# Optimization experiments

Measured on AMD Instinct MI355X. Metric: run time of the kernel, lower is better.

## Reference

```python
import jax, jax.numpy as jnp
import numpy as np
import math

B, S, H = 8, 1024, 768
NH = 12
DH = H // NH


def _linear(x, W, b):
    # torch Linear: y = x @ W.T + b, W: [out, in]
    return jnp.einsum('bsd,ed->bse', x, W) + b


def _split_heads(x):
    # [B,S,H] -> [B,NH,S,DH]
    b, s, _ = x.shape
    return x.reshape(b, s, NH, DH).transpose(0, 2, 1, 3)


def _attend(q, k, v):
    # q,k,v: [B,NH,S,DH]
    scores = jnp.einsum('bhqd,bhkd->bhqk', q, k) / math.sqrt(DH)
    probs = jax.nn.softmax(scores, axis=-1)
    ctx = jnp.einsum('bhqk,bhkd->bhqd', probs, v)
    b, h, s, d = ctx.shape
    return ctx.transpose(0, 2, 1, 3).reshape(b, s, h * d)


def setup_inputs() -> dict:
    key = jax.random.key(0)
    ks = jax.random.split(key, 20)
    sc = 1.0 / math.sqrt(H)
    inp = {
        'hidden_statesx': jax.random.normal(ks[0], (B, S, H), jnp.float32),
        'hidden_statesy': jax.random.normal(ks[1], (B, S, H), jnp.float32),
    }
    names = ['Wq', 'Wk', 'Wv', 'Wo', 'Wqd', 'Wkd', 'Wvd', 'Wod']
    for i, n in enumerate(names):
        inp[n] = jax.random.normal(ks[2 + i], (H, H), jnp.float32) * sc
        inp['b' + n[1:]] = jnp.zeros((H,), jnp.float32)
    inp['w11'] = jnp.full((1,), 0.5, jnp.float32)
    inp['w12'] = jnp.full((1,), 0.5, jnp.float32)
    inp['w21'] = jnp.full((1,), 0.5, jnp.float32)
    inp['w22'] = jnp.full((1,), 0.5, jnp.float32)
    return inp


def reference(hidden_statesx, hidden_statesy,
              Wq, bq, Wk, bk, Wv, bv, Wo, bo,
              Wqd, bqd, Wkd, bkd, Wvd, bvd, Wod, bod,
              w11, w12, w21, w22):
    q = _split_heads(_linear(hidden_statesx, Wq, bq))
    k = _split_heads(_linear(hidden_statesx, Wk, bk))
    v = _split_heads(_linear(hidden_statesx, Wv, bv))
    qd = _split_heads(_linear(hidden_statesy, Wqd, bqd))
    kd = _split_heads(_linear(hidden_statesy, Wkd, bkd))
    vd = _split_heads(_linear(hidden_statesy, Wvd, bvd))

    # self-attention on x and y streams
    attention_sx = _linear(_attend(q, k, v), Wo, bo)
    attention_sy = _linear(_attend(qd, kd, vd), Wod, bod)
    # cross attentions (mba mode)
    attention_cx = _linear(_attend(q, kd, vd), Wo, bo)
    attention_cy = _linear(_attend(qd, k, v), Wod, bod)

    attention_sx = w11 * attention_sx + w12 * attention_cx
    attention_sy = w21 * attention_sy + w22 * attention_cy
    return attention_sx, attention_sy
```

## Files before the change

### kernel.cpp

```cpp
#include <hip/hip_runtime.h>

typedef __bf16 bf16;
typedef __bf16 bf16x8 __attribute__((ext_vector_type(8)));
typedef float f32x4 __attribute__((ext_vector_type(4)));

#define HD 768
#define ELTS 6291456
#define WELTS 589824

__device__ __forceinline__ void gld_lds16(const bf16* g, bf16* l) {
  __builtin_amdgcn_global_load_lds((const __attribute__((address_space(1))) void*)g,
                                   (__attribute__((address_space(3))) void*)l, 16, 0, 0);
}

__device__ __forceinline__ float rdscalar(const void* p, int f) {
  return f ? (float)((const bf16*)p)[0] : ((const float*)p)[0];
}

__device__ __forceinline__ float exp2fast(float x) {
#if __has_builtin(__builtin_amdgcn_exp2f)
  return __builtin_amdgcn_exp2f(x);
#else
  return __builtin_exp2f(x);
#endif
}

__global__ void probe_dtype(const unsigned int* __restrict__ x, int* flag) {
  const int t = threadIdx.x;
  int bad = 0;
#pragma unroll
  for (int i = 0; i < 4; ++i) {
    unsigned int wd = x[t * 4 + i];
    unsigned int e0 = (wd >> 7) & 0xFF;
    unsigned int e1 = (wd >> 23) & 0xFF;
    bad += (e0 >= 134) + (e1 >= 134);
  }
  unsigned long long m = __ballot(bad > 0);
  if (t == 0) *flag = (m == 0ULL) ? 1 : 0;
}

struct CvtArgs {
  const float* src[20];
  bf16* dst[20];
  int n[20];
  const int* flag;
};
__global__ __launch_bounds__(256) void convert_inputs(CvtArgs a) {
  if (*a.flag) return;
  const int seg = blockIdx.y;
  const float* s = a.src[seg];
  bf16* d = a.dst[seg];
  const int n4 = a.n[seg] >> 2;
  for (int i = blockIdx.x * blockDim.x + threadIdx.x; i < n4; i += gridDim.x * blockDim.x) {
    f32x4 v = *(const f32x4*)(s + i * 4);
    bf16 o[4];
#pragma unroll
    for (int e = 0; e < 4; ++e) o[e] = (bf16)v[e];
    *(unsigned long long*)(d + i * 4) = *(unsigned long long*)o;
  }
}

struct GemmArgs {
  const void* A[6];
  const void* Ac[6];
  const void* W[6];
  const void* Wc[6];
  const void* bias[6];
  const void* biasc[6];
  const void* s0[6];
  const void* s1[6];
  void* C[6];
  float cmul[6];
  int c_fixed[6];
  int vt[6];
  int ext_w[6];
  long long out_elem_off[6];
  const int* flag;
};

__global__ __launch_bounds__(256) void gemm_bt(GemmArgs args) {
  const int g = blockIdx.z;
  const int f = *args.flag;
  const bool c_bf = args.c_fixed[g] || f;
  const bool w_f32 = (!f) && args.ext_w[g];
  const bf16* __restrict__ A = (const bf16*)(f ? args.A[g] : args.Ac[g]);
  const void* __restrict__ Wp = f ? args.W[g] : args.Wc[g];
  const void* __restrict__ bias = f ? args.bias[g] : args.biasc[g];
  bf16* Cb = (bf16*)args.C[g] + args.out_elem_off[g];
  float* Cf = (float*)args.C[g] + args.out_elem_off[g];
  float bscale = 1.0f;
  if (args.s0[g]) bscale = rdscalar(args.s0[g], f) + rdscalar(args.s1[g], f);
  const float cmul = args.cmul[g];

  const int m0 = blockIdx.x * 128;
  const int n0 = blockIdx.y * 128;
  const int t = threadIdx.x;
  const int lane = t & 63;
  const int w = t >> 6;
  const int wm = (w >> 1) * 64, wn = (w & 1) * 64;

  __shared__ __attribute__((aligned(16))) bf16 As[128 * 64];
  __shared__ __attribute__((aligned(16))) bf16 Bs[128 * 64];

  f32x4 acc[4][4] = {};

  const int row_s = t >> 3, slot_s = t & 7;
  const int gswz = (slot_s ^ (row_s & 7)) << 3;

  const int fr = lane & 15;
  const int l4 = lane >> 4;
  const int sR0 = ((l4) ^ (fr & 7)) << 3;
  const int sR1 = ((4 + l4) ^ (fr & 7)) << 3;

  for (int kb = 0; kb < 12; ++kb) {
    const int k0 = kb * 64;
#pragma unroll
    for (int i = 0; i < 4; ++i) {
      const int row = row_s + i * 32;
      gld_lds16(A + (size_t)(m0 + row) * HD + k0 + gswz, As + (t + i * 256) * 8);
    }
    if (!w_f32) {
#pragma unroll
      for (int i = 0; i < 4; ++i) {
        const int row = row_s + i * 32;
        gld_lds16((const bf16*)Wp + (size_t)(n0 + row) * HD + k0 + gswz, Bs + (t + i * 256) * 8);
      }
    } else {
      const float* Wf = (const float*)Wp;
#pragma unroll
      for (int i = 0; i < 4; ++i) {
        const int row = row_s + i * 32;
        const size_t src = (size_t)(n0 + row) * HD + k0 + gswz;
        f32x4 u0 = *(const f32x4*)(Wf + src), u1 = *(const f32x4*)(Wf + src + 4);
        bf16x8 v;
#pragma unroll
        for (int e = 0; e < 4; ++e) { v[e] = (bf16)u0[e]; v[e + 4] = (bf16)u1[e]; }
        *(bf16x8*)(Bs + (t + i * 256) * 8) = v;
      }
    }
    __syncthreads();
#pragma unroll
    for (int kk = 0; kk < 2; ++kk) {
      const int sR = kk ? sR1 : sR0;
      bf16x8 af[4], bfr[4];
#pragma unroll
      for (int mi = 0; mi < 4; ++mi)
        af[mi] = *(const bf16x8*)(As + (wm + mi * 16 + fr) * 64 + sR);
#pragma unroll
      for (int ni = 0; ni < 4; ++ni)
        bfr[ni] = *(const bf16x8*)(Bs + (wn + ni * 16 + fr) * 64 + sR);
#pragma unroll
      for (int mi = 0; mi < 4; ++mi)
#pragma unroll
        for (int ni = 0; ni < 4; ++ni)
          acc[mi][ni] = __builtin_amdgcn_mfma_f32_16x16x32_bf16(af[mi], bfr[ni], acc[mi][ni], 0, 0, 0);
    }
    __syncthreads();
  }

  const int rq = (lane >> 4) * 4;
  const int is_vt = args.vt[g];
#pragma unroll
  for (int ni = 0; ni < 4; ++ni) {
    const int col = n0 + wn + ni * 16 + fr;
    const float bv = (w_f32 ? ((const float*)bias)[col]
                            : (float)((const bf16*)bias)[col]) * bscale;
#pragma unroll
    for (int mi = 0; mi < 4; ++mi) {
      const int row = m0 + wm + mi * 16 + rq;
      if (is_vt) {
        const int bb = row >> 10, s = row & 1023;
        const int hh = col >> 6, d = col & 63;
        bf16 tmp[4];
#pragma unroll
        for (int r = 0; r < 4; ++r) tmp[r] = (bf16)((acc[mi][ni][r] + bv) * cmul);
        *(unsigned long long*)(Cb + (((size_t)(bb * 12 + hh)) << 16) + (d << 10) + s) =
            *(const unsigned long long*)tmp;
      } else {
#pragma unroll
        for (int r = 0; r < 4; ++r) {
          const float val = (acc[mi][ni][r] + bv) * cmul;
          if (c_bf) Cb[(size_t)(row + r) * HD + col] = (bf16)val;
          else      Cf[(size_t)(row + r) * HD + col] = val;
        }
      }
    }
  }
}

__global__ __launch_bounds__(256, 4) void attn_mba(
    const bf16* __restrict__ Q, const bf16* __restrict__ Kx, const bf16* __restrict__ Vtx,
    const bf16* __restrict__ Qd, const bf16* __restrict__ Kd, const bf16* __restrict__ Vtd,
    const void* w11, const void* w12, const void* w21, const void* w22,
    bf16* ctxX, bf16* ctxY, const int* flag) {
  const int linear = blockIdx.x + (blockIdx.y << 4);
  const int swz = (linear & 7) * 192 + (linear >> 3);
  const int qb = swz & 15;
  const int bh = swz >> 4;
  const int b = bh / 12;
  const int f = *flag;

  const float wgtX[2] = {rdscalar(w11, f), rdscalar(w12, f)};
  const float wgtY[2] = {rdscalar(w22, f), rdscalar(w21, f)};

  const size_t tok0 = (size_t)b * 1024;
  const size_t vbase = (size_t)bh * 65536;
  const int fcol = (bh - b * 12) * 64;
  const int q0 = qb * 64;

  __shared__ __attribute__((aligned(16))) bf16 smem[16384];
  bf16* Ks = smem;
  bf16* Vs = smem + 8192;

  const int t = threadIdx.x, lane = t & 63, w = t >> 6;
  const int l15 = lane & 15, l4 = lane >> 4;

  const int g0 = t >> 3, slot0 = t & 7;
  const int g1 = g0 + 32;
  const int gs = (slot0 ^ (g0 & 7)) << 3;
  const int kp0 = (g0 & 32) + ((g0 & 12) << 1) + ((g0 & 16) >> 2) + (g0 & 3);
  const int kp1 = (g1 & 32) + ((g1 & 12) << 1) + ((g1 & 16) >> 2) + (g1 & 3);
  const size_t koffg0 = (tok0 + kp0) * HD + fcol + gs;
  const size_t koffg1 = (tok0 + kp1) * HD + fcol + gs;
  const size_t voffg0 = vbase + (size_t)g0 * 1024 + gs;
  const size_t voffg1 = vbase + (size_t)g1 * 1024 + gs;

  auto stage = [&](int nit) {
    const bf16* Kc = nit < 16 ? Kx : Kd;
    const bf16* Vc = nit < 16 ? Vtx : Vtd;
    const int kt64 = (nit & 15) * 64;
    bf16* Kb = Ks + (nit & 1) * 4096;
    bf16* Vb = Vs + (nit & 1) * 4096;
    gld_lds16(Kc + koffg0 + (size_t)kt64 * HD, Kb + t * 8);
    gld_lds16(Kc + koffg1 + (size_t)kt64 * HD, Kb + (t + 256) * 8);
    gld_lds16(Vc + voffg0 + kt64, Vb + t * 8);
    gld_lds16(Vc + voffg1 + kt64, Vb + (t + 256) * 8);
  };

  stage(0);

  const int qrow = w * 16 + l15;
  const bf16* qp0 = Q  + (tok0 + q0 + qrow) * HD + fcol;
  const bf16* qp1 = Qd + (tok0 + q0 + qrow) * HD + fcol;
  bf16x8 qf[2][2];
  qf[0][0] = *(const bf16x8*)(qp0 + (l4 << 3));
  qf[0][1] = *(const bf16x8*)(qp0 + ((4 + l4) << 3));
  qf[1][0] = *(const bf16x8*)(qp1 + (l4 << 3));
  qf[1][1] = *(const bf16x8*)(qp1 + ((4 + l4) << 3));

  const int kbase = l15 * 64 + ((l4 ^ (l15 & 7)) << 3);

  __syncthreads();

  f32x4 mixX[4] = {}, mixY[4] = {};
  f32x4 oacc[2][4] = {};
  f32x4 lsum[2] = {};

  for (int it = 0; it < 32; ++it) {
    if (it) __syncthreads();
    if (it + 1 < 32) stage(it + 1);
    const bf16* Kb = Ks + (it & 1) * 4096;
    const bf16* Vb = Vs + (it & 1) * 4096;

#pragma unroll
    for (int s2 = 0; s2 < 2; ++s2) {
      f32x4 sv[4];
      __builtin_amdgcn_s_setprio(1);
#pragma unroll
      for (int mi = 0; mi < 4; ++mi) {
        bf16x8 kf0 = *(const bf16x8*)(Kb + (kbase + mi * 1024));
        bf16x8 kf1 = *(const bf16x8*)(Kb + ((kbase + mi * 1024) ^ 32));
        f32x4 s = {};
        s = __builtin_amdgcn_mfma_f32_16x16x32_bf16(kf0, qf[s2][0], s, 0, 0, 0);
        s = __builtin_amdgcn_mfma_f32_16x16x32_bf16(kf1, qf[s2][1], s, 0, 0, 0);
        sv[mi] = s;
      }
      __builtin_amdgcn_s_setprio(0);

      f32x4 ls = lsum[s2];
#pragma unroll
      for (int mi = 0; mi < 4; ++mi) {
        f32x4 e;
#pragma unroll
        for (int r = 0; r < 4; ++r) e[r] = exp2fast(sv[mi][r]);
        sv[mi] = e;
        ls += e;
      }
      lsum[s2] = ls;

#pragma unroll
      for (int c = 0; c < 2; ++c) {
        bf16x8 pf;
#pragma unroll
        for (int j = 0; j < 8; ++j)
          pf[j] = (bf16)sv[2 * c + (j >> 2)][j & 3];
        __builtin_amdgcn_s_setprio(1);
#pragma unroll
        for (int mi = 0; mi < 4; ++mi) {
          bf16x8 vf = *(const bf16x8*)(Vb + ((kbase + mi * 1024) ^ (c << 5)));
          oacc[s2][mi] = __builtin_amdgcn_mfma_f32_16x16x32_bf16(vf, pf, oacc[s2][mi], 0, 0, 0);
        }
        __builtin_amdgcn_s_setprio(0);
      }
    }

    if ((it & 15) == 15) {
      const int ph = it >> 4;
      float l0 = (lsum[0][0] + lsum[0][1]) + (lsum[0][2] + lsum[0][3]);
      float l1 = (lsum[1][0] + lsum[1][1]) + (lsum[1][2] + lsum[1][3]);
      l0 += __shfl_xor(l0, 16); l0 += __shfl_xor(l0, 32);
      l1 += __shfl_xor(l1, 16); l1 += __shfl_xor(l1, 32);
      const float scX = wgtX[ph] / l0;
      const float scY = wgtY[ph] / l1;
#pragma unroll
      for (int mi = 0; mi < 4; ++mi) {
#pragma unroll
        for (int r = 0; r < 4; ++r) {
          mixX[mi][r] += scX * oacc[0][mi][r];
          mixY[mi][r] += scY * oacc[1][mi][r];
        }
        oacc[0][mi] = f32x4{};
        oacc[1][mi] = f32x4{};
      }
      lsum[0] = f32x4{};
      lsum[1] = f32x4{};
    }
  }

  __syncthreads();
  bf16* TX = smem;
  bf16* TY = smem + 4608;
#pragma unroll
  for (int mi = 0; mi < 4; ++mi)
#pragma unroll
    for (int r = 0; r < 4; ++r) {
      TX[qrow * 72 + mi * 16 + l4 * 4 + r] = (bf16)mixX[mi][r];
      TY[qrow * 72 + mi * 16 + l4 * 4 + r] = (bf16)mixY[mi][r];
    }
  __syncthreads();
#pragma unroll
  for (int i = 0; i < 2; ++i) {
    const int q = t + i * 256;
    const int g = q >> 3, dc = (q & 7) * 8;
    *(bf16x8*)(ctxX + (tok0 + q0 + g) * HD + fcol + dc) = *(const bf16x8*)(TX + g * 72 + dc);
    *(bf16x8*)(ctxY + (tok0 + q0 + g) * HD + fcol + dc) = *(const bf16x8*)(TY + g * 72 + dc);
  }
}

extern "C" void kernel_launch(void* const* d_in, const int* in_sizes, int n_in,
                              void* d_out, int out_size, void* d_ws, size_t ws_size,
                              hipStream_t stream) {
  (void)in_sizes; (void)n_in; (void)out_size;
  const void* x = d_in[0];
  const void* y = d_in[1];

  bf16* ws = (bf16*)d_ws;
  bf16* Qb   = ws + 0ull * ELTS;
  bf16* Kb   = ws + 1ull * ELTS;
  bf16* Vtb  = ws + 2ull * ELTS;
  bf16* Qdb  = ws + 3ull * ELTS;
  bf16* Kdb  = ws + 4ull * ELTS;
  bf16* Vtdb = ws + 5ull * ELTS;
  bf16* ctxX = Qb;
  bf16* ctxY = Qdb;
  int* flag = (int*)(ws + 6ull * ELTS);

  const size_t extra_elems = 6ull * ELTS + 32 + 2ull * WELTS + 2 * 768;
  const bool big_ws = ws_size >= extra_elems * sizeof(bf16);
  bf16* extraW = ws + 6ull * ELTS + 32;
  bf16* extraB = extraW + 2ull * WELTS;

  bf16* cb = (bf16*)d_out;
  bf16* xb = cb;
  bf16* yb = cb + (size_t)ELTS;
  bf16* Wcv = cb + 2ull * ELTS;
  bf16* bcv = Wcv + 6ull * WELTS;

  probe_dtype<<<dim3(1), dim3(64), 0, stream>>>((const unsigned int*)x, flag);

  CvtArgs ca;
  int nseg = 14;
  {
    const int wsrc[6] = {2, 4, 6, 10, 12, 14};
    ca.src[0] = (const float*)x;  ca.dst[0] = xb;  ca.n[0] = ELTS;
    ca.src[1] = (const float*)y;  ca.dst[1] = yb;  ca.n[1] = ELTS;
    for (int i = 0; i < 6; ++i) {
      ca.src[2 + i] = (const float*)d_in[wsrc[i]];
      ca.dst[2 + i] = Wcv + (size_t)i * WELTS;
      ca.n[2 + i] = WELTS;
      ca.src[8 + i] = (const float*)d_in[wsrc[i] + 1];
      ca.dst[8 + i] = bcv + (size_t)i * 768;
      ca.n[8 + i] = 768;
    }
    if (big_ws) {
      ca.src[14] = (const float*)d_in[8];  ca.dst[14] = extraW;         ca.n[14] = WELTS;
      ca.src[15] = (const float*)d_in[16]; ca.dst[15] = extraW + WELTS; ca.n[15] = WELTS;
      ca.src[16] = (const float*)d_in[9];  ca.dst[16] = extraB;         ca.n[16] = 768;
      ca.src[17] = (const float*)d_in[17]; ca.dst[17] = extraB + 768;   ca.n[17] = 768;
      nseg = 18;
    }
    ca.flag = flag;
  }
  convert_inputs<<<dim3(512, nseg), dim3(256), 0, stream>>>(ca);

  GemmArgs gq;
  {
    const void* A6[6]  = {x, x, x, y, y, y};
    const void* Ac6[6] = {xb, xb, xb, yb, yb, yb};
    const int di[6] = {2, 4, 6, 10, 12, 14};
    bf16* C6[6] = {Qb, Kb, Vtb, Qdb, Kdb, Vtdb};
    for (int i = 0; i < 6; ++i) {
      gq.A[i] = A6[i]; gq.Ac[i] = Ac6[i];
      gq.W[i] = d_in[di[i]]; gq.Wc[i] = Wcv + (size_t)i * WELTS;
      gq.bias[i] = d_in[di[i] + 1]; gq.biasc[i] = bcv + (size_t)i * 768;
      gq.s0[i] = nullptr; gq.s1[i] = nullptr; gq.C[i] = C6[i];
      gq.cmul[i] = (i == 0 || i == 3) ? 0.18033688011112042f : 1.0f;
      gq.c_fixed[i] = 1; gq.ext_w[i] = 0; gq.out_elem_off[i] = 0;
      gq.vt[i] = (i == 2 || i == 5) ? 1 : 0;
    }
    gq.flag = flag;
  }
  gemm_bt<<<dim3(64, 6, 6), dim3(256), 0, stream>>>(gq);

  attn_mba<<<dim3(16, 96), dim3(256), 0, stream>>>(
      Qb, Kb, Vtb, Qdb, Kdb, Vtdb, d_in[18], d_in[19], d_in[20], d_in[21],
      ctxX, ctxY, flag);

  GemmArgs gp;
  for (int i = 0; i < 6; ++i) {
    gp.A[i] = ctxX; gp.Ac[i] = ctxX;
    gp.W[i] = d_in[8]; gp.Wc[i] = d_in[8];
    gp.bias[i] = d_in[9]; gp.biasc[i] = d_in[9];
    gp.s0[i] = d_in[18]; gp.s1[i] = d_in[19]; gp.C[i] = d_out;
    gp.cmul[i] = 1.0f; gp.c_fixed[i] = 0; gp.vt[i] = 0;
    gp.ext_w[i] = 1; gp.out_elem_off[i] = 0;
  }
  gp.A[1] = ctxY; gp.Ac[1] = ctxY;
  gp.W[1] = d_in[16]; gp.Wc[1] = d_in[16];
  gp.bias[1] = d_in[17]; gp.biasc[1] = d_in[17];
  gp.s0[1] = d_in[20]; gp.s1[1] = d_in[21];
  gp.out_elem_off[1] = (long long)ELTS;
  if (big_ws) {
    gp.Wc[0] = extraW;         gp.biasc[0] = extraB;       gp.ext_w[0] = 0;
    gp.Wc[1] = extraW + WELTS; gp.biasc[1] = extraB + 768; gp.ext_w[1] = 0;
  }
  gp.flag = flag;
  gemm_bt<<<dim3(64, 6, 2), dim3(256), 0, stream>>>(gp);
}
```

Before: 396.7 us.

## Split K/V waits with vmcnt barriers and share K/V fragments across both query streams

Replaces the per-iteration __syncthreads with explicit s_waitcnt vmcnt plus s_barrier pairs. QK^T can now start once only the K tile has landed, while the V tile and the next stage's loads are still in flight. The inner two-stream loop is merged so each K and V LDS fragment is read once and fed to MFMAs for both the x and y query streams. This halves LDS fragment reads and gives the scheduler more independent MFMA chains. The hand-counted vmcnt values depend on the exact number and order of outstanding global loads, and the extra barrier adds a sync point per iteration.

```diff
diff --git a/kernel.cpp b/kernel.cpp
--- a/kernel.cpp
+++ b/kernel.cpp
@@ -237,77 +237,81 @@
     gld_lds16(Vc + voffg1 + kt64, Vb + (t + 256) * 8);
   };
 
-  stage(0);
-
   const int qrow = w * 16 + l15;
   const bf16* qp0 = Q  + (tok0 + q0 + qrow) * HD + fcol;
   const bf16* qp1 = Qd + (tok0 + q0 + qrow) * HD + fcol;
-  bf16x8 qf[2][2];
-  qf[0][0] = *(const bf16x8*)(qp0 + (l4 << 3));
-  qf[0][1] = *(const bf16x8*)(qp0 + ((4 + l4) << 3));
-  qf[1][0] = *(const bf16x8*)(qp1 + (l4 << 3));
-  qf[1][1] = *(const bf16x8*)(qp1 + ((4 + l4) << 3));
+  bf16x8 qf00 = *(const bf16x8*)(qp0 + (l4 << 3));
+  bf16x8 qf01 = *(const bf16x8*)(qp0 + ((4 + l4) << 3));
+  bf16x8 qf10 = *(const bf16x8*)(qp1 + (l4 << 3));
+  bf16x8 qf11 = *(const bf16x8*)(qp1 + ((4 + l4) << 3));
+
+  stage(0);
 
   const int kbase = l15 * 64 + ((l4 ^ (l15 & 7)) << 3);
-
-  __syncthreads();
 
   f32x4 mixX[4] = {}, mixY[4] = {};
   f32x4 oacc[2][4] = {};
-  f32x4 lsum[2] = {};
+  f32x4 ls0 = {}, ls1 = {};
 
   for (int it = 0; it < 32; ++it) {
-    if (it) __syncthreads();
+    asm volatile("s_waitcnt vmcnt(2)" ::: "memory");
+    __builtin_amdgcn_s_barrier();
     if (it + 1 < 32) stage(it + 1);
+
     const bf16* Kb = Ks + (it & 1) * 4096;
     const bf16* Vb = Vs + (it & 1) * 4096;
 
-#pragma unroll
-    for (int s2 = 0; s2 < 2; ++s2) {
-      f32x4 sv[4];
-      __builtin_amdgcn_s_setprio(1);
+    f32x4 sv0[4], sv1[4];
+    __builtin_amdgcn_s_setprio(1);
+#pragma unroll
+    for (int mi = 0; mi < 4; ++mi) {
+      bf16x8 kf0 = *(const bf16x8*)(Kb + (kbase + mi * 1024));
+      bf16x8 kf1 = *(const bf16x8*)(Kb + ((kbase + mi * 1024) ^ 32));
+      f32x4 a = {}, c = {};
+      a = __builtin_amdgcn_mfma_f32_16x16x32_bf16(kf0, qf00, a, 0, 0, 0);
+      a = __builtin_amdgcn_mfma_f32_16x16x32_bf16(kf1, qf01, a, 0, 0, 0);
+      c = __builtin_amdgcn_mfma_f32_16x16x32_bf16(kf0, qf10, c, 0, 0, 0);
+      c = __builtin_amdgcn_mfma_f32_16x16x32_bf16(kf1, qf11, c, 0, 0, 0);
+      sv0[mi] = a; sv1[mi] = c;
+    }
+    __builtin_amdgcn_s_setprio(0);
+
+#pragma unroll
+    for (int mi = 0; mi < 4; ++mi) {
+      f32x4 e0, e1;
+#pragma unroll
+      for (int r = 0; r < 4; ++r) { e0[r] = exp2fast(sv0[mi][r]); e1[r] = exp2fast(sv1[mi][r]); }
+      sv0[mi] = e0; sv1[mi] = e1;
+      ls0 += e0; ls1 += e1;
+    }
+    bf16x8 pf0[2], pf1[2];
+#pragma unroll
+    for (int c = 0; c < 2; ++c)
+#pragma unroll
+      for (int j = 0; j < 8; ++j) {
+        pf0[c][j] = (bf16)sv0[2 * c + (j >> 2)][j & 3];
+        pf1[c][j] = (bf16)sv1[2 * c + (j >> 2)][j & 3];
+      }
+
+    if (it < 31) asm volatile("s_waitcnt vmcnt(4)" ::: "memory");
+    else         asm volatile("s_waitcnt vmcnt(0)" ::: "memory");
+    __builtin_amdgcn_s_barrier();
+
+    __builtin_amdgcn_s_setprio(1);
+#pragma unroll
+    for (int c = 0; c < 2; ++c)
 #pragma unroll
       for (int mi = 0; mi < 4; ++mi) {
-        bf16x8 kf0 = *(const bf16x8*)(Kb + (kbase + mi * 1024));
-        bf16x8 kf1 = *(const bf16x8*)(Kb + ((kbase + mi * 1024) ^ 32));
-        f32x4 s = {};
-        s = __builtin_amdgcn_mfma_f32_16x16x32_bf16(kf0, qf[s2][0], s, 0, 0, 0);
-        s = __builtin_amdgcn_mfma_f32_16x16x32_bf16(kf1, qf[s2][1], s, 0, 0, 0);
-        sv[mi] = s;
-      }
-      __builtin_amdgcn_s_setprio(0);
-
-      f32x4 ls = lsum[s2];
-#pragma unroll
-      for (int mi = 0; mi < 4; ++mi) {
-        f32x4 e;
-#pragma unroll
-        for (int r = 0; r < 4; ++r) e[r] = exp2fast(sv[mi][r]);
-        sv[mi] = e;
-        ls += e;
-      }
-      lsum[s2] = ls;
-
-#pragma unroll
-      for (int c = 0; c < 2; ++c) {
-        bf16x8 pf;
-#pragma unroll
-        for (int j = 0; j < 8; ++j)
-          pf[j] = (bf16)sv[2 * c + (j >> 2)][j & 3];
-        __builtin_amdgcn_s_setprio(1);
-#pragma unroll
-        for (int mi = 0; mi < 4; ++mi) {
-          bf16x8 vf = *(const bf16x8*)(Vb + ((kbase + mi * 1024) ^ (c << 5)));
-          oacc[s2][mi] = __builtin_amdgcn_mfma_f32_16x16x32_bf16(vf, pf, oacc[s2][mi], 0, 0, 0);
-        }
-        __builtin_amdgcn_s_setprio(0);
-      }
-    }
+        bf16x8 vf = *(const bf16x8*)(Vb + ((kbase + mi * 1024) ^ (c << 5)));
+        oacc[0][mi] = __builtin_amdgcn_mfma_f32_16x16x32_bf16(vf, pf0[c], oacc[0][mi], 0, 0, 0);
+        oacc[1][mi] = __builtin_amdgcn_mfma_f32_16x16x32_bf16(vf, pf1[c], oacc[1][mi], 0, 0, 0);
+      }
+    __builtin_amdgcn_s_setprio(0);
 
     if ((it & 15) == 15) {
       const int ph = it >> 4;
-      float l0 = (lsum[0][0] + lsum[0][1]) + (lsum[0][2] + lsum[0][3]);
-      float l1 = (lsum[1][0] + lsum[1][1]) + (lsum[1][2] + lsum[1][3]);
+      float l0 = (ls0[0] + ls0[1]) + (ls0[2] + ls0[3]);
+      float l1 = (ls1[0] + ls1[1]) + (ls1[2] + ls1[3]);
       l0 += __shfl_xor(l0, 16); l0 += __shfl_xor(l0, 32);
       l1 += __shfl_xor(l1, 16); l1 += __shfl_xor(l1, 32);
       const float scX = wgtX[ph] / l0;
@@ -322,8 +326,8 @@
         oacc[0][mi] = f32x4{};
         oacc[1][mi] = f32x4{};
       }
-      lsum[0] = f32x4{};
-      lsum[1] = f32x4{};
+      ls0 = f32x4{};
+      ls1 = f32x4{};
     }
   }
 
```

New measurement: 416.5 us. 5.0% more time.
